# Optimization experiments

Hardware: AMD Instinct MI355X
Metric: run time of the kernel (lower is better)

The kernel has to match this reference:

```python
import jax, jax.numpy as jnp
import numpy as np

B, NNODE, D = 128, 64, 64          # graphs, nodes per graph, invariant feat dim
N = B * NNODE                      # 8192 nodes
E = B * NNODE * (NNODE - 1)        # 516096 directed edges (fully connected per graph)


def _silu(x):
    return x * jax.nn.sigmoid(x)


def _ln(x, w, b, eps=1e-5):
    mu = jnp.mean(x, axis=-1, keepdims=True)
    var = jnp.var(x, axis=-1, keepdims=True)
    return (x - mu) / jnp.sqrt(var + eps) * w + b


def setup_inputs() -> dict:
    key = jax.random.key(0)
    ks = jax.random.split(key, 12)
    # node -> graph assignment, sorted
    batch = np.repeat(np.arange(B), NNODE)
    # fully-connected directed edges within each graph (i != j)
    idx = np.arange(NNODE)
    s, d = np.meshgrid(idx, idx, indexing='ij')
    m = s != d
    s, d = s[m], d[m]
    off = (np.arange(B) * NNODE)[:, None]
    src = (s[None, :] + off).ravel()
    dst = (d[None, :] + off).ravel()
    E_idx = jnp.asarray(np.stack([src, dst]), dtype=jnp.int32)
    return dict(
        batch=jnp.asarray(batch, jnp.int32),
        X=jax.random.normal(ks[0], (N, 3), jnp.float32),
        H=jax.random.normal(ks[1], (N, D), jnp.float32),
        E_idx=E_idx,
        x_norm_w=jnp.ones((1, 1), jnp.float32),
        q_w1=jax.random.normal(ks[2], (D, D), jnp.float32) * 0.05,
        q_w2=jax.random.normal(ks[3], (D, D), jnp.float32) * 0.05,
        kv_w1=jax.random.normal(ks[4], (D + 1, 2 * D), jnp.float32) * 0.05,
        kv_w2=jax.random.normal(ks[5], (2 * D, 2 * D), jnp.float32) * 0.05,
        qn_w=jnp.ones((D,), jnp.float32), qn_b=jnp.zeros((D,), jnp.float32),
        kn_w=jnp.ones((D,), jnp.float32), kn_b=jnp.zeros((D,), jnp.float32),
        phx_w1=jax.random.normal(ks[6], (D, D), jnp.float32) * 0.05,
        phx_w2=jax.random.normal(ks[7], (D, 1), jnp.float32) * 0.05,
        phh_w1=jax.random.normal(ks[8], (D, D), jnp.float32) * 0.05,
        phh_b1=jnp.zeros((D,), jnp.float32),
        phh_w2=jax.random.normal(ks[9], (D, D), jnp.float32) * 0.05,
        phh_b2=jnp.zeros((D,), jnp.float32),
    )


def reference(batch, X, H, E_idx, x_norm_w, q_w1, q_w2, kv_w1, kv_w2,
              qn_w, qn_b, kn_w, kn_b, phx_w1, phx_w2,
              phh_w1, phh_b1, phh_w2, phh_b2):
    src, dst = E_idx[0], E_idx[1]
    # ---- E3Norm: scale positions by per-graph mean norm ----
    norm = jnp.linalg.norm(X, axis=-1, keepdims=True)                 # [N,1]
    cnt = jax.ops.segment_sum(jnp.ones((N,), X.dtype), batch, num_segments=B)
    mean_norm = jax.ops.segment_sum(norm, batch, num_segments=B) / cnt[:, None]
    Xn = x_norm_w * X / (mean_norm[batch] + 1e-5)                     # [N,3]
    # ---- edge gathers + MLPs ----
    Q = _silu(H[dst] @ q_w1) @ q_w2                                   # [E,D]
    rel = Xn[src] - Xn[dst]                                           # [E,3]
    rel_dist = jnp.sum(rel * rel, axis=-1, keepdims=True)             # [E,1]
    X_rel_norm = rel / (1.0 + jnp.sqrt(rel_dist + 1e-8))
    kv_in = jnp.concatenate([rel_dist, H[src]], axis=-1)              # [E,D+1]
    kv = _silu(kv_in @ kv_w1) @ kv_w2                                 # [E,2D]
    K, V = kv[:, :D], kv[:, D:]
    Q = _ln(Q, qn_w, qn_b)
    K = _ln(K, kn_w, kn_b)
    # ---- scatter softmax over incoming edges of dst ----
    scores = jnp.sum(Q * K, axis=-1) / jnp.sqrt(jnp.asarray(D, X.dtype))  # [E]
    m = jax.ops.segment_max(scores, dst, num_segments=N)
    e = jnp.exp(scores - m[dst])
    s = jax.ops.segment_sum(e, dst, num_segments=N)
    alpha = e / s[dst]                                                # [E]
    att = alpha[:, None] * V                                          # [E,D]
    # ---- scatter-sum aggregations ----
    A = jax.ops.segment_sum(att, dst, num_segments=N)                 # [N,D]
    AH = jax.ops.segment_sum(att * H[dst], dst, num_segments=N)       # [N,D]
    phx = _silu(att @ phx_w1) @ phx_w2                                # [E,1]
    X_out = Xn + jax.ops.segment_sum(X_rel_norm * phx, dst, num_segments=N)
    H_out = H + (_silu((A * AH) @ phh_w1 + phh_b1) @ phh_w2 + phh_b2)
    return X_out, H_out
```

## Files before the change

kernel.cpp:

```cpp
#include <hip/hip_runtime.h>
#include <math.h>

#define NB     128
#define NNODE  64
#define NTOT   8192
#define DIM    64
#define PSTR   136
#define WS72   72

typedef __bf16 bf16x8 __attribute__((ext_vector_type(8)));
typedef float  f32x4  __attribute__((ext_vector_type(4)));

__device__ __forceinline__ float frcp(float x) {
    return __builtin_amdgcn_rcpf(x);
}

__device__ __forceinline__ float silu_f(float x) {
    return x * frcp(1.0f + __expf(-x));
}

__device__ __forceinline__ unsigned short bf16bits(float f) {
    return __builtin_bit_cast(unsigned short, (__bf16)f);
}

__device__ __forceinline__ bf16x8 to_bf16x8(const float* v) {
    bf16x8 o;
    #pragma unroll
    for (int j = 0; j < 8; ++j) o[j] = (__bf16)v[j];
    return o;
}

__device__ __forceinline__ float wsum(float v) {
    #pragma unroll
    for (int m = 1; m < 64; m <<= 1) v += __shfl_xor(v, m, 64);
    return v;
}

template<int CTRL>
__device__ __forceinline__ float dpp_add(float v) {
    const int r = __builtin_amdgcn_update_dpp(
        0, __builtin_bit_cast(int, v), CTRL, 0xF, 0xF, true);
    return v + __builtin_bit_cast(float, r);
}
__device__ __forceinline__ float row_sum16(float v) {
    v = dpp_add<0x111>(v);
    v = dpp_add<0x112>(v);
    v = dpp_add<0x114>(v);
    v = dpp_add<0x118>(v);
    return v;
}
__device__ __forceinline__ float bcast15(float v) {
    return __builtin_bit_cast(float,
        __builtin_amdgcn_ds_swizzle(__builtin_bit_cast(int, v), 0x01F0));
}

__global__ __launch_bounds__(256) void k0_prep(
        const float* __restrict__ kvw2, const float* __restrict__ phxw1,
        const float* __restrict__ X, const float* __restrict__ xw,
        const float* __restrict__ qw1, const float* __restrict__ qw2,
        const float* __restrict__ kvw1,
        const float* __restrict__ phh1, const float* __restrict__ phh2,
        unsigned short* __restrict__ w2x, float* __restrict__ Xn4,
        unsigned short* __restrict__ qw1T, unsigned short* __restrict__ qw2T,
        unsigned short* __restrict__ kvw1T,
        unsigned short* __restrict__ phh1T, unsigned short* __restrict__ phh2T) {
    const int k = blockIdx.x;
    const int T = threadIdx.x;
    if (T < 128) {
        w2x[T*PSTR + k] = bf16bits(kvw2[k*128 + T]);
    } else if (T < 192) {
        const int n2 = T - 128;
        float acc = 0.f;
        #pragma unroll 8
        for (int j = 0; j < 64; ++j)
            acc += kvw2[k*128 + 64 + j] * phxw1[j*64 + n2];
        w2x[(128 + n2)*PSTR + k] = bf16bits(acc);
    } else {
        const int L = T - 192;
        const int n = k*64 + L;
        const float x0 = X[n*3+0], x1 = X[n*3+1], x2 = X[n*3+2];
        const float nm = sqrtf(x0*x0 + x1*x1 + x2*x2);
        const float mean = wsum(nm) * (1.0f/64.0f);
        const float sc = xw[0] * frcp(mean + 1e-5f);
        float4 o; o.x = x0*sc; o.y = x1*sc; o.z = x2*sc; o.w = 0.f;
        *(float4*)&Xn4[n*4] = o;
    }
    if (k < 64) {
        if (T < 128) kvw1T[T*WS72 + k] = bf16bits(kvw1[(1+k)*128 + T]);
    } else {
        const int kk = k - 64;
        if (T < 64)       qw1T[T*WS72 + kk]        = bf16bits(qw1[kk*64 + T]);
        else if (T < 128) qw2T[(T-64)*WS72 + kk]   = bf16bits(qw2[kk*64 + (T-64)]);
        else if (T < 192) phh1T[(T-128)*WS72 + kk] = bf16bits(phh1[kk*64 + (T-128)]);
        else              phh2T[(T-192)*WS72 + kk] = bf16bits(phh2[kk*64 + (T-192)]);
    }
}

__global__ __launch_bounds__(64) void k2_node(
        const float* __restrict__ H,
        const unsigned short* __restrict__ wbase,
        const float* __restrict__ qnw, const float* __restrict__ qnb,
        float* __restrict__ Qn, unsigned short* __restrict__ Ptb) {
    const int tile = blockIdx.x >> 1, role = blockIdx.x & 1;
    const int nb = tile * 16;
    const int L = threadIdx.x, q = L >> 4, m = L & 15;
    __shared__ __align__(16) unsigned short zb[16*WS72];

    bf16x8 hf[2];
    #pragma unroll
    for (int ks = 0; ks < 2; ++ks) {
        float v[8];
        *(float4*)&v[0] = *(const float4*)&H[(size_t)(nb + m)*64 + ks*32 + q*8];
        *(float4*)&v[4] = *(const float4*)&H[(size_t)(nb + m)*64 + ks*32 + q*8 + 4];
        hf[ks] = to_bf16x8(v);
    }

    f32x4 acc[4];
    if (role == 1) {
        const unsigned short* kvw1T = wbase + 128*WS72;
        #pragma unroll
        for (int ph = 0; ph < 2; ++ph) {
            #pragma unroll
            for (int ct = 0; ct < 4; ++ct) acc[ct] = (f32x4){0.f,0.f,0.f,0.f};
            #pragma unroll
            for (int ks = 0; ks < 2; ++ks)
                #pragma unroll
                for (int ct = 0; ct < 4; ++ct) {
                    const bf16x8 b = *(const bf16x8*)&kvw1T[(ph*64 + ct*16 + m)*WS72 + ks*32 + q*8];
                    acc[ct] = __builtin_amdgcn_mfma_f32_16x16x32_bf16(hf[ks], b, acc[ct], 0, 0, 0);
                }
            #pragma unroll
            for (int ct = 0; ct < 4; ++ct)
                #pragma unroll
                for (int r = 0; r < 4; ++r)
                    Ptb[(size_t)(nb + q*4 + r)*PSTR + ph*64 + ct*16 + m]
                        = bf16bits(acc[ct][r]);
        }
        return;
    }

    #pragma unroll
    for (int ct = 0; ct < 4; ++ct) acc[ct] = (f32x4){0.f,0.f,0.f,0.f};
    #pragma unroll
    for (int ks = 0; ks < 2; ++ks)
        #pragma unroll
        for (int ct = 0; ct < 4; ++ct) {
            const bf16x8 b = *(const bf16x8*)&wbase[(ct*16 + m)*WS72 + ks*32 + q*8];
            acc[ct] = __builtin_amdgcn_mfma_f32_16x16x32_bf16(hf[ks], b, acc[ct], 0, 0, 0);
        }
    #pragma unroll
    for (int ct = 0; ct < 4; ++ct)
        #pragma unroll
        for (int r = 0; r < 4; ++r)
            zb[(q*4 + r)*WS72 + ct*16 + m] = bf16bits(silu_f(acc[ct][r]));

    bf16x8 zf[2];
    #pragma unroll
    for (int ks = 0; ks < 2; ++ks)
        zf[ks] = *(const bf16x8*)&zb[m*WS72 + ks*32 + q*8];
    const unsigned short* qw2T = wbase + 64*WS72;
    #pragma unroll
    for (int ct = 0; ct < 4; ++ct) acc[ct] = (f32x4){0.f,0.f,0.f,0.f};
    #pragma unroll
    for (int ks = 0; ks < 2; ++ks)
        #pragma unroll
        for (int ct = 0; ct < 4; ++ct) {
            const bf16x8 b = *(const bf16x8*)&qw2T[(ct*16 + m)*WS72 + ks*32 + q*8];
            acc[ct] = __builtin_amdgcn_mfma_f32_16x16x32_bf16(zf[ks], b, acc[ct], 0, 0, 0);
        }
    float qnwv[4], qnbv[4];
    #pragma unroll
    for (int ct = 0; ct < 4; ++ct) { qnwv[ct] = qnw[ct*16+m]; qnbv[ct] = qnb[ct*16+m]; }
    #pragma unroll
    for (int r = 0; r < 4; ++r) {
        float s1 = 0.f, s2 = 0.f;
        #pragma unroll
        for (int ct = 0; ct < 4; ++ct) {
            const float z = acc[ct][r];
            s1 += z; s2 = fmaf(z, z, s2);
        }
        #pragma unroll
        for (int sh = 1; sh < 16; sh <<= 1) {
            s1 += __shfl_xor(s1, sh, 64);
            s2 += __shfl_xor(s2, sh, 64);
        }
        const float mu = s1 * (1.0f/64.0f);
        const float rstd = rsqrtf(s2 * (1.0f/64.0f) - mu*mu + 1e-5f);
        const int row = nb + q*4 + r;
        #pragma unroll
        for (int ct = 0; ct < 4; ++ct)
            Qn[(size_t)row*64 + ct*16 + m] = (acc[ct][r] - mu)*rstd*qnwv[ct] + qnbv[ct];
    }
}

__global__ __launch_bounds__(256, 3) void k3_edge(
        const float* __restrict__ Xn4, const float* __restrict__ Qn,
        const unsigned short* __restrict__ Ptb,
        const unsigned short* __restrict__ w2x,
        const float* __restrict__ kvw1,
        const float* __restrict__ knw, const float* __restrict__ knb,
        const float* __restrict__ pxw2,
        float* __restrict__ Abuf, float* __restrict__ Xout) {
    const int bid = blockIdx.x;
    const int g = bid >> 3, dgrp = bid & 7;
    const int T = threadIdx.x, w = T >> 6, L = T & 63;
    const int q = L >> 4, m = L & 15;
    const int pair = w >> 1, half = w & 1;

    __shared__ __align__(16) unsigned short sw2[128*PSTR];
    __shared__ __align__(16) float sXn[64][4];
    __shared__ __align__(16) float sQn[8][64];
    __shared__ __align__(16) float sxr[4][32][4];
    __shared__ float w0s[128];
    __shared__ float knws[64], knbs[64], pxs[64];
    __shared__ float sred[2][2][2];
    __shared__ float sA[2][64];
    __shared__ float sX[2][4];

    {
        const uint4* s1 = (const uint4*)w2x;
        uint4* d1 = (uint4*)sw2;
        #pragma unroll
        for (int it = 0; it < 9; ++it) {
            const int idx = T + 256*it;
            if (idx < 128*PSTR/8) d1[idx] = s1[idx];
        }
        const float* qsrc = Qn + ((size_t)g*64 + dgrp*8)*64;
        for (int idx = T; idx < 512; idx += 256)
            sQn[idx >> 6][idx & 63] = qsrc[idx];
        if (T < 64) *(float4*)&sXn[T][0] = *(const float4*)&Xn4[(g*64 + T)*4];
        if (T < 128) w0s[T] = kvw1[T];
        if (T < 64)            knws[T]       = knw[T];
        else if (T < 128)      knbs[T - 64]  = knb[T - 64];
        else if (T < 192)      pxs[T - 128]  = pxw2[T - 128];
    }
    __syncthreads();

    const unsigned short* PtG = Ptb + (size_t)g*64*PSTR;
    const unsigned short* Gw  = w2x + 128*PSTR;
    const float mflag = (m == 15) ? 1.0f : 0.0f;

    #pragma unroll 1
    for (int i = 0; i < 4; ++i) {
        const int dql = i*2 + pair;
        const int dl  = dgrp*8 + dql;
        const int d   = g*64 + dl;

        if (L < 32) {
            const int row = half*32 + L;
            const float4 xs  = *(const float4*)&sXn[row][0];
            const float4 xdv = *(const float4*)&sXn[dl][0];
            const float r0 = xs.x - xdv.x, r1 = xs.y - xdv.y, r2 = xs.z - xdv.z;
            const float rd = r0*r0 + r1*r1 + r2*r2;
            const float inv = frcp(1.0f + sqrtf(rd + 1e-8f));
            float4 o; o.x = r0*inv; o.y = r1*inv; o.z = r2*inv; o.w = rd;
            *(float4*)&sxr[w][L][0] = o;
        }
        asm volatile("s_waitcnt lgkmcnt(0)" ::: "memory");

        bf16x8 af[2][4];
        float rdv[2];
        #pragma unroll
        for (int rt = 0; rt < 2; ++rt) rdv[rt] = sxr[w][rt*16 + m][3];
        #pragma unroll
        for (int ks = 0; ks < 4; ++ks) {
            float w0v[8];
            *(float4*)&w0v[0] = *(const float4*)&w0s[ks*32 + q*8];
            *(float4*)&w0v[4] = *(const float4*)&w0s[ks*32 + q*8 + 4];
            #pragma unroll
            for (int rt = 0; rt < 2; ++rt) {
                const int row = half*32 + rt*16 + m;
                const bf16x8 pb = *(const bf16x8*)&PtG[(size_t)row*PSTR + ks*32 + q*8];
                bf16x8 o;
                #pragma unroll
                for (int j = 0; j < 8; ++j) {
                    const float pf = (float)pb[j];
                    o[j] = (__bf16)silu_f(fmaf(rdv[rt], w0v[j], pf));
                }
                af[rt][ks] = o;
            }
        }

        f32x4 acc[4][2];

        #pragma unroll
        for (int ct = 0; ct < 4; ++ct)
            #pragma unroll
            for (int rt = 0; rt < 2; ++rt)
                acc[ct][rt] = (f32x4){0.f, 0.f, 0.f, 0.f};
        #pragma unroll
        for (int ks = 0; ks < 4; ++ks)
            #pragma unroll
            for (int ct = 0; ct < 4; ++ct) {
                const bf16x8 b = *(const bf16x8*)&sw2[(ct*16 + m)*PSTR + ks*32 + q*8];
                #pragma unroll
                for (int rt = 0; rt < 2; ++rt)
                    acc[ct][rt] = __builtin_amdgcn_mfma_f32_16x16x32_bf16(
                                      af[rt][ks], b, acc[ct][rt], 0, 0, 0);
            }

        float qdw[4], Sqdw = 0.f, Sqdb = 0.f;
        #pragma unroll
        for (int ct = 0; ct < 4; ++ct) {
            const float qd = sQn[dql][ct*16 + m];
            qdw[ct] = qd * knws[ct*16 + m];
            Sqdw += qdw[ct];
            Sqdb += qd * knbs[ct*16 + m];
        }
        Sqdw = row_sum16(Sqdw);
        Sqdb = row_sum16(Sqdb);
        float sc[2][4];
        #pragma unroll
        for (int rt = 0; rt < 2; ++rt)
            #pragma unroll
            for (int r = 0; r < 4; ++r) {
                float s1 = 0.f, s2 = 0.f, skq = 0.f;
                #pragma unroll
                for (int ct = 0; ct < 4; ++ct) {
                    const float kv = acc[ct][rt][r];
                    s1 += kv; s2 = fmaf(kv, kv, s2); skq = fmaf(kv, qdw[ct], skq);
                }
                s1  = row_sum16(s1);
                s2  = row_sum16(s2);
                skq = row_sum16(skq);
                const float mu = s1 * (1.0f/64.0f);
                const float rstd = rsqrtf(s2 * (1.0f/64.0f) - mu*mu + 1e-5f);
                float scv = (rstd * (skq - mu*Sqdw) + Sqdb) * 0.125f;
                scv = bcast15(scv);
                const int row_g = half*32 + rt*16 + q*4 + r;
                sc[rt][r] = (row_g == dl) ? -1e30f : scv;
            }

        float mx = -1e30f;
        #pragma unroll
        for (int rt = 0; rt < 2; ++rt)
            #pragma unroll
            for (int r = 0; r < 4; ++r) mx = fmaxf(mx, sc[rt][r]);
        mx = fmaxf(mx, __shfl_xor(mx, 16, 64));
        mx = fmaxf(mx, __shfl_xor(mx, 32, 64));
        float al[2][4], S = 0.f;
        #pragma unroll
        for (int rt = 0; rt < 2; ++rt)
            #pragma unroll
            for (int r = 0; r < 4; ++r) {
                al[rt][r] = __expf(sc[rt][r] - mx);
                S += al[rt][r];
            }
        S += __shfl_xor(S, 16, 64);
        S += __shfl_xor(S, 32, 64);
        if (L == 0) { sred[pair][half][0] = mx; sred[pair][half][1] = S; }
        __syncthreads();
        {
            const float mo = sred[pair][half^1][0];
            const float So = sred[pair][half^1][1];
            const float M  = fmaxf(mx, mo);
            const float es = __expf(mx - M);
            const float eo = __expf(mo - M);
            const float alf = es * frcp(S*es + So*eo);
            #pragma unroll
            for (int rt = 0; rt < 2; ++rt)
                #pragma unroll
                for (int r = 0; r < 4; ++r) al[rt][r] *= alf;
        }

        #pragma unroll
        for (int ct = 0; ct < 4; ++ct)
            #pragma unroll
            for (int rt = 0; rt < 2; ++rt)
                acc[ct][rt] = (f32x4){0.f, 0.f, 0.f, 0.f};
        #pragma unroll
        for (int ks = 0; ks < 4; ++ks)
            #pragma unroll
            for (int ct = 0; ct < 4; ++ct) {
                const bf16x8 b = *(const bf16x8*)&sw2[(64 + ct*16 + m)*PSTR + ks*32 + q*8];
                #pragma unroll
                for (int rt = 0; rt < 2; ++rt)
                    acc[ct][rt] = __builtin_amdgcn_mfma_f32_16x16x32_bf16(
                                      af[rt][ks], b, acc[ct][rt], 0, 0, 0);
            }
        float p[4];
        #pragma unroll
        for (int ct = 0; ct < 4; ++ct) {
            float pv = 0.f;
            #pragma unroll
            for (int rt = 0; rt < 2; ++rt)
                #pragma unroll
                for (int r = 0; r < 4; ++r)
                    pv = fmaf(al[rt][r], acc[ct][rt][r], pv);
            pv += __shfl_xor(pv, 16, 64);
            pv += __shfl_xor(pv, 32, 64);
            p[ct] = pv;
        }

        #pragma unroll
        for (int ct = 0; ct < 4; ++ct)
            #pragma unroll
            for (int rt = 0; rt < 2; ++rt)
                acc[ct][rt] = (f32x4){0.f, 0.f, 0.f, 0.f};
        #pragma unroll
        for (int ks = 0; ks < 4; ++ks)
            #pragma unroll
            for (int ct = 0; ct < 4; ++ct) {
                const bf16x8 b = *(const bf16x8*)&Gw[(size_t)(ct*16 + m)*PSTR + ks*32 + q*8];
                #pragma unroll
                for (int rt = 0; rt < 2; ++rt)
                    acc[ct][rt] = __builtin_amdgcn_mfma_f32_16x16x32_bf16(
                                      af[rt][ks], b, acc[ct][rt], 0, 0, 0);
            }

        float pxc[4];
        #pragma unroll
        for (int ct = 0; ct < 4; ++ct) pxc[ct] = pxs[ct*16 + m];
        float xa0 = 0.f, xa1 = 0.f, xa2 = 0.f;
        #pragma unroll
        for (int rt = 0; rt < 2; ++rt)
            #pragma unroll
            for (int r = 0; r < 4; ++r) {
                float ph = 0.f;
                #pragma unroll
                for (int ct = 0; ct < 4; ++ct)
                    ph = fmaf(silu_f(al[rt][r] * acc[ct][rt][r]), pxc[ct], ph);
                ph = row_sum16(ph) * mflag;
                const float4 xr = *(const float4*)&sxr[w][rt*16 + q*4 + r][0];
                xa0 = fmaf(ph, xr.x, xa0);
                xa1 = fmaf(ph, xr.y, xa1);
                xa2 = fmaf(ph, xr.z, xa2);
            }
        xa0 += __shfl_xor(xa0, 16, 64); xa0 += __shfl_xor(xa0, 32, 64);
        xa1 += __shfl_xor(xa1, 16, 64); xa1 += __shfl_xor(xa1, 32, 64);
        xa2 += __shfl_xor(xa2, 16, 64); xa2 += __shfl_xor(xa2, 32, 64);

        if (half == 1) {
            if (q == 0)
                #pragma unroll
                for (int ct = 0; ct < 4; ++ct) sA[pair][ct*16 + m] = p[ct];
            if (L == 15) {
                sX[pair][0] = xa0; sX[pair][1] = xa1; sX[pair][2] = xa2;
            }
        }
        __syncthreads();
        if (half == 0) {
            if (q == 0)
                #pragma unroll
                for (int ct = 0; ct < 4; ++ct)
                    Abuf[(size_t)d*64 + ct*16 + m] = p[ct] + sA[pair][ct*16 + m];
            if (L == 15) {
                const float4 xdv = *(const float4*)&sXn[dl][0];
                Xout[(size_t)d*3 + 0] = xdv.x + xa0 + sX[pair][0];
                Xout[(size_t)d*3 + 1] = xdv.y + xa1 + sX[pair][1];
                Xout[(size_t)d*3 + 2] = xdv.z + xa2 + sX[pair][2];
            }
        }
    }
}

__global__ __launch_bounds__(64) void k4_hout(
        const float* __restrict__ H, const float* __restrict__ Abuf,
        const unsigned short* __restrict__ wbase,
        const float* __restrict__ b1, const float* __restrict__ b2,
        float* __restrict__ Hout) {
    const int nb = blockIdx.x * 16;
    const int L = threadIdx.x, q = L >> 4, m = L & 15;
    __shared__ __align__(16) unsigned short zb[16*WS72];

    bf16x8 uf[2];
    #pragma unroll
    for (int ks = 0; ks < 2; ++ks) {
        const size_t base = (size_t)(nb + m)*64 + ks*32 + q*8;
        float a[8], h[8], v[8];
        *(float4*)&a[0] = *(const float4*)&Abuf[base];
        *(float4*)&a[4] = *(const float4*)&Abuf[base + 4];
        *(float4*)&h[0] = *(const float4*)&H[base];
        *(float4*)&h[4] = *(const float4*)&H[base + 4];
        #pragma unroll
        for (int j = 0; j < 8; ++j) v[j] = a[j]*a[j]*h[j];
        uf[ks] = to_bf16x8(v);
    }

    f32x4 acc[4];
    #pragma unroll
    for (int ct = 0; ct < 4; ++ct) acc[ct] = (f32x4){0.f,0.f,0.f,0.f};
    #pragma unroll
    for (int ks = 0; ks < 2; ++ks)
        #pragma unroll
        for (int ct = 0; ct < 4; ++ct) {
            const bf16x8 b = *(const bf16x8*)&wbase[(ct*16 + m)*WS72 + ks*32 + q*8];
            acc[ct] = __builtin_amdgcn_mfma_f32_16x16x32_bf16(uf[ks], b, acc[ct], 0, 0, 0);
        }
    #pragma unroll
    for (int ct = 0; ct < 4; ++ct) {
        const float bv = b1[ct*16 + m];
        #pragma unroll
        for (int r = 0; r < 4; ++r)
            zb[(q*4 + r)*WS72 + ct*16 + m] = bf16bits(silu_f(acc[ct][r] + bv));
    }

    bf16x8 zf[2];
    #pragma unroll
    for (int ks = 0; ks < 2; ++ks)
        zf[ks] = *(const bf16x8*)&zb[m*WS72 + ks*32 + q*8];
    const unsigned short* phh2T = wbase + 64*WS72;
    #pragma unroll
    for (int ct = 0; ct < 4; ++ct) acc[ct] = (f32x4){0.f,0.f,0.f,0.f};
    #pragma unroll
    for (int ks = 0; ks < 2; ++ks)
        #pragma unroll
        for (int ct = 0; ct < 4; ++ct) {
            const bf16x8 b = *(const bf16x8*)&phh2T[(ct*16 + m)*WS72 + ks*32 + q*8];
            acc[ct] = __builtin_amdgcn_mfma_f32_16x16x32_bf16(zf[ks], b, acc[ct], 0, 0, 0);
        }
    #pragma unroll
    for (int ct = 0; ct < 4; ++ct) {
        const float bv = b2[ct*16 + m];
        #pragma unroll
        for (int r = 0; r < 4; ++r) {
            const size_t idx = (size_t)(nb + q*4 + r)*64 + ct*16 + m;
            Hout[idx] = H[idx] + acc[ct][r] + bv;
        }
    }
}

extern "C" void kernel_launch(void* const* d_in, const int* in_sizes, int n_in,
                              void* d_out, int out_size, void* d_ws, size_t ws_size,
                              hipStream_t stream) {
    const float* X    = (const float*)d_in[1];
    const float* H    = (const float*)d_in[2];
    const float* xw   = (const float*)d_in[4];
    const float* qw1  = (const float*)d_in[5];
    const float* qw2  = (const float*)d_in[6];
    const float* kvw1 = (const float*)d_in[7];
    const float* kvw2 = (const float*)d_in[8];
    const float* qnw  = (const float*)d_in[9];
    const float* qnb  = (const float*)d_in[10];
    const float* knw  = (const float*)d_in[11];
    const float* knb  = (const float*)d_in[12];
    const float* pxw1 = (const float*)d_in[13];
    const float* pxw2 = (const float*)d_in[14];
    const float* phw1 = (const float*)d_in[15];
    const float* phb1 = (const float*)d_in[16];
    const float* phw2 = (const float*)d_in[17];
    const float* phb2 = (const float*)d_in[18];

    float* out = (float*)d_out;
    char*  ws  = (char*)d_ws;

    size_t off = 0;
    float* Xn4 = (float*)(ws + off);          off += (size_t)NTOT*4*4;
    float* Qn  = (float*)(ws + off);          off += (size_t)NTOT*64*4;
    unsigned short* Ptb = (unsigned short*)(ws + off); off += (size_t)NTOT*PSTR*2;
    float* Ab  = (float*)(ws + off);          off += (size_t)NTOT*64*4;
    unsigned short* w2x   = (unsigned short*)(ws + off); off += (size_t)192*PSTR*2;
    unsigned short* qw1T  = (unsigned short*)(ws + off); off += (size_t)64*WS72*2;
    unsigned short* qw2T  = (unsigned short*)(ws + off); off += (size_t)64*WS72*2;
    unsigned short* kvw1T = (unsigned short*)(ws + off); off += (size_t)128*WS72*2;
    unsigned short* phh1T = (unsigned short*)(ws + off); off += (size_t)64*WS72*2;
    unsigned short* phh2T = (unsigned short*)(ws + off); off += (size_t)64*WS72*2;

    k0_prep<<<128, 256, 0, stream>>>(kvw2, pxw1, X, xw, qw1, qw2, kvw1,
                                     phw1, phw2, w2x, Xn4,
                                     qw1T, qw2T, kvw1T, phh1T, phh2T);
    k2_node<<<1024, 64, 0, stream>>>(H, qw1T, qnw, qnb, Qn, Ptb);
    k3_edge<<<1024, 256, 0, stream>>>(Xn4, Qn, Ptb, w2x, kvw1, knw, knb,
                                      pxw2, Ab, out);
    k4_hout<<<512, 64, 0, stream>>>(H, Ab, phh1T, phb1, phb2, out + NTOT*3);
}
```

Before: 173.1 us.

## Fuse H-output MLP into edge kernel and restructure MFMA accumulators per column tile

Removes the separate k4_hout kernel: each edge block keeps its 8 aggregated A rows in shared memory as bf16 and runs the phh MLP with one wave after a block barrier, so the global A buffer round trip and one launch disappear. The three MFMA stages now loop per column tile with a small accumulator and fold reductions in immediately, which cuts register pressure and allows launch bounds of 4 blocks. The Qn and Xn shared staging is dropped in favour of direct global loads. The added tail wastes half of a wave (q<2) and serialises on one wave, and A is now rounded to bf16 before squaring.

```diff
diff --git a/kernel.cpp b/kernel.cpp
--- a/kernel.cpp
+++ b/kernel.cpp
@@ -193,14 +193,17 @@
     }
 }
 
-__global__ __launch_bounds__(256, 3) void k3_edge(
+__global__ __launch_bounds__(256, 4) void k3_edge(
         const float* __restrict__ Xn4, const float* __restrict__ Qn,
         const unsigned short* __restrict__ Ptb,
         const unsigned short* __restrict__ w2x,
         const float* __restrict__ kvw1,
         const float* __restrict__ knw, const float* __restrict__ knb,
         const float* __restrict__ pxw2,
-        float* __restrict__ Abuf, float* __restrict__ Xout) {
+        const unsigned short* __restrict__ phhT,
+        const float* __restrict__ phb1, const float* __restrict__ phb2,
+        const float* __restrict__ H,
+        float* __restrict__ Hout, float* __restrict__ Xout) {
     const int bid = blockIdx.x;
     const int g = bid >> 3, dgrp = bid & 7;
     const int T = threadIdx.x, w = T >> 6, L = T & 63;
@@ -208,9 +211,8 @@
     const int pair = w >> 1, half = w & 1;
 
     __shared__ __align__(16) unsigned short sw2[128*PSTR];
-    __shared__ __align__(16) float sXn[64][4];
-    __shared__ __align__(16) float sQn[8][64];
     __shared__ __align__(16) float sxr[4][32][4];
+    __shared__ __align__(16) unsigned short sAb[8*WS72];
     __shared__ float w0s[128];
     __shared__ float knws[64], knbs[64], pxs[64];
     __shared__ float sred[2][2][2];
@@ -225,10 +227,6 @@
             const int idx = T + 256*it;
             if (idx < 128*PSTR/8) d1[idx] = s1[idx];
         }
-        const float* qsrc = Qn + ((size_t)g*64 + dgrp*8)*64;
-        for (int idx = T; idx < 512; idx += 256)
-            sQn[idx >> 6][idx & 63] = qsrc[idx];
-        if (T < 64) *(float4*)&sXn[T][0] = *(const float4*)&Xn4[(g*64 + T)*4];
         if (T < 128) w0s[T] = kvw1[T];
         if (T < 64)            knws[T]       = knw[T];
         else if (T < 128)      knbs[T - 64]  = knb[T - 64];
@@ -246,10 +244,15 @@
         const int dl  = dgrp*8 + dql;
         const int d   = g*64 + dl;
 
+        float qdv[4];
+        #pragma unroll
+        for (int ct = 0; ct < 4; ++ct)
+            qdv[ct] = Qn[(size_t)d*64 + ct*16 + m];
+
         if (L < 32) {
             const int row = half*32 + L;
-            const float4 xs  = *(const float4*)&sXn[row][0];
-            const float4 xdv = *(const float4*)&sXn[dl][0];
+            const float4 xs  = *(const float4*)&Xn4[(g*64 + row)*4];
+            const float4 xdv = *(const float4*)&Xn4[(g*64 + dl)*4];
             const float r0 = xs.x - xdv.x, r1 = xs.y - xdv.y, r2 = xs.z - xdv.z;
             const float rd = r0*r0 + r1*r1 + r2*r2;
             const float inv = frcp(1.0f + sqrtf(rd + 1e-8f));
@@ -281,48 +284,54 @@
             }
         }
 
-        f32x4 acc[4][2];
-
-        #pragma unroll
-        for (int ct = 0; ct < 4; ++ct)
-            #pragma unroll
-            for (int rt = 0; rt < 2; ++rt)
-                acc[ct][rt] = (f32x4){0.f, 0.f, 0.f, 0.f};
-        #pragma unroll
-        for (int ks = 0; ks < 4; ++ks)
-            #pragma unroll
-            for (int ct = 0; ct < 4; ++ct) {
-                const bf16x8 b = *(const bf16x8*)&sw2[(ct*16 + m)*PSTR + ks*32 + q*8];
-                #pragma unroll
-                for (int rt = 0; rt < 2; ++rt)
-                    acc[ct][rt] = __builtin_amdgcn_mfma_f32_16x16x32_bf16(
-                                      af[rt][ks], b, acc[ct][rt], 0, 0, 0);
-            }
-
         float qdw[4], Sqdw = 0.f, Sqdb = 0.f;
         #pragma unroll
         for (int ct = 0; ct < 4; ++ct) {
-            const float qd = sQn[dql][ct*16 + m];
-            qdw[ct] = qd * knws[ct*16 + m];
+            qdw[ct] = qdv[ct] * knws[ct*16 + m];
             Sqdw += qdw[ct];
-            Sqdb += qd * knbs[ct*16 + m];
+            Sqdb += qdv[ct] * knbs[ct*16 + m];
         }
         Sqdw = row_sum16(Sqdw);
         Sqdb = row_sum16(Sqdb);
+
+        float s1a[2][4], s2a[2][4], skqa[2][4];
+        #pragma unroll
+        for (int rt = 0; rt < 2; ++rt)
+            #pragma unroll
+            for (int r = 0; r < 4; ++r) { s1a[rt][r]=0.f; s2a[rt][r]=0.f; skqa[rt][r]=0.f; }
+
+        #pragma unroll
+        for (int ct = 0; ct < 4; ++ct) {
+            f32x4 acc[2];
+            acc[0] = (f32x4){0.f,0.f,0.f,0.f};
+            acc[1] = (f32x4){0.f,0.f,0.f,0.f};
+            #pragma unroll
+            for (int ks = 0; ks < 4; ++ks) {
+                const bf16x8 b = *(const bf16x8*)&sw2[(ct*16 + m)*PSTR + ks*32 + q*8];
+                #pragma unroll
+                for (int rt = 0; rt < 2; ++rt)
+                    acc[rt] = __builtin_amdgcn_mfma_f32_16x16x32_bf16(
+                                  af[rt][ks], b, acc[rt], 0, 0, 0);
+            }
+            #pragma unroll
+            for (int rt = 0; rt < 2; ++rt)
+                #pragma unroll
+                for (int r = 0; r < 4; ++r) {
+                    const float kv = acc[rt][r];
+                    s1a[rt][r] += kv;
+                    s2a[rt][r] = fmaf(kv, kv, s2a[rt][r]);
+                    skqa[rt][r] = fmaf(kv, qdw[ct], skqa[rt][r]);
+                }
+        }
+
         float sc[2][4];
         #pragma unroll
         for (int rt = 0; rt < 2; ++rt)
             #pragma unroll
             for (int r = 0; r < 4; ++r) {
-                float s1 = 0.f, s2 = 0.f, skq = 0.f;
-                #pragma unroll
-                for (int ct = 0; ct < 4; ++ct) {
-                    const float kv = acc[ct][rt][r];
-                    s1 += kv; s2 = fmaf(kv, kv, s2); skq = fmaf(kv, qdw[ct], skq);
-                }
-                s1  = row_sum16(s1);
-                s2  = row_sum16(s2);
-                skq = row_sum16(skq);
+                const float s1 = row_sum16(s1a[rt][r]);
+                const float s2 = row_sum16(s2a[rt][r]);
+                const float skq = row_sum16(skqa[rt][r]);
                 const float mu = s1 * (1.0f/64.0f);
                 const float rstd = rsqrtf(s2 * (1.0f/64.0f) - mu*mu + 1e-5f);
                 float scv = (rstd * (skq - mu*Sqdw) + Sqdb) * 0.125f;
@@ -363,64 +372,63 @@
                 for (int r = 0; r < 4; ++r) al[rt][r] *= alf;
         }
 
-        #pragma unroll
-        for (int ct = 0; ct < 4; ++ct)
+        float p[4];
+        #pragma unroll
+        for (int ct = 0; ct < 4; ++ct) {
+            f32x4 acc[2];
+            acc[0] = (f32x4){0.f,0.f,0.f,0.f};
+            acc[1] = (f32x4){0.f,0.f,0.f,0.f};
+            #pragma unroll
+            for (int ks = 0; ks < 4; ++ks) {
+                const bf16x8 b = *(const bf16x8*)&sw2[(64 + ct*16 + m)*PSTR + ks*32 + q*8];
+                #pragma unroll
+                for (int rt = 0; rt < 2; ++rt)
+                    acc[rt] = __builtin_amdgcn_mfma_f32_16x16x32_bf16(
+                                  af[rt][ks], b, acc[rt], 0, 0, 0);
+            }
+            float pv = 0.f;
             #pragma unroll
             for (int rt = 0; rt < 2; ++rt)
-                acc[ct][rt] = (f32x4){0.f, 0.f, 0.f, 0.f};
-        #pragma unroll
-        for (int ks = 0; ks < 4; ++ks)
-            #pragma unroll
-            for (int ct = 0; ct < 4; ++ct) {
-                const bf16x8 b = *(const bf16x8*)&sw2[(64 + ct*16 + m)*PSTR + ks*32 + q*8];
-                #pragma unroll
-                for (int rt = 0; rt < 2; ++rt)
-                    acc[ct][rt] = __builtin_amdgcn_mfma_f32_16x16x32_bf16(
-                                      af[rt][ks], b, acc[ct][rt], 0, 0, 0);
-            }
-        float p[4];
-        #pragma unroll
-        for (int ct = 0; ct < 4; ++ct) {
-            float pv = 0.f;
-            #pragma unroll
-            for (int rt = 0; rt < 2; ++rt)
                 #pragma unroll
                 for (int r = 0; r < 4; ++r)
-                    pv = fmaf(al[rt][r], acc[ct][rt][r], pv);
+                    pv = fmaf(al[rt][r], acc[rt][r], pv);
             pv += __shfl_xor(pv, 16, 64);
             pv += __shfl_xor(pv, 32, 64);
             p[ct] = pv;
         }
 
-        #pragma unroll
-        for (int ct = 0; ct < 4; ++ct)
+        float phsum[2][4];
+        #pragma unroll
+        for (int rt = 0; rt < 2; ++rt)
+            #pragma unroll
+            for (int r = 0; r < 4; ++r) phsum[rt][r] = 0.f;
+        #pragma unroll
+        for (int ct = 0; ct < 4; ++ct) {
+            f32x4 acc[2];
+            acc[0] = (f32x4){0.f,0.f,0.f,0.f};
+            acc[1] = (f32x4){0.f,0.f,0.f,0.f};
+            #pragma unroll
+            for (int ks = 0; ks < 4; ++ks) {
+                const bf16x8 b = *(const bf16x8*)&Gw[(size_t)(ct*16 + m)*PSTR + ks*32 + q*8];
+                #pragma unroll
+                for (int rt = 0; rt < 2; ++rt)
+                    acc[rt] = __builtin_amdgcn_mfma_f32_16x16x32_bf16(
+                                  af[rt][ks], b, acc[rt], 0, 0, 0);
+            }
+            const float px = pxs[ct*16 + m];
             #pragma unroll
             for (int rt = 0; rt < 2; ++rt)
-                acc[ct][rt] = (f32x4){0.f, 0.f, 0.f, 0.f};
-        #pragma unroll
-        for (int ks = 0; ks < 4; ++ks)
-            #pragma unroll
-            for (int ct = 0; ct < 4; ++ct) {
-                const bf16x8 b = *(const bf16x8*)&Gw[(size_t)(ct*16 + m)*PSTR + ks*32 + q*8];
-                #pragma unroll
-                for (int rt = 0; rt < 2; ++rt)
-                    acc[ct][rt] = __builtin_amdgcn_mfma_f32_16x16x32_bf16(
-                                      af[rt][ks], b, acc[ct][rt], 0, 0, 0);
-            }
-
-        float pxc[4];
-        #pragma unroll
-        for (int ct = 0; ct < 4; ++ct) pxc[ct] = pxs[ct*16 + m];
+                #pragma unroll
+                for (int r = 0; r < 4; ++r)
+                    phsum[rt][r] = fmaf(silu_f(al[rt][r] * acc[rt][r]), px, phsum[rt][r]);
+        }
+
         float xa0 = 0.f, xa1 = 0.f, xa2 = 0.f;
         #pragma unroll
         for (int rt = 0; rt < 2; ++rt)
             #pragma unroll
             for (int r = 0; r < 4; ++r) {
-                float ph = 0.f;
-                #pragma unroll
-                for (int ct = 0; ct < 4; ++ct)
-                    ph = fmaf(silu_f(al[rt][r] * acc[ct][rt][r]), pxc[ct], ph);
-                ph = row_sum16(ph) * mflag;
+                const float ph = row_sum16(phsum[rt][r]) * mflag;
                 const float4 xr = *(const float4*)&sxr[w][rt*16 + q*4 + r][0];
                 xa0 = fmaf(ph, xr.x, xa0);
                 xa1 = fmaf(ph, xr.y, xa1);
@@ -443,79 +451,79 @@
             if (q == 0)
                 #pragma unroll
                 for (int ct = 0; ct < 4; ++ct)
-                    Abuf[(size_t)d*64 + ct*16 + m] = p[ct] + sA[pair][ct*16 + m];
+                    sAb[dql*WS72 + ct*16 + m] =
+                        bf16bits(p[ct] + sA[pair][ct*16 + m]);
             if (L == 15) {
-                const float4 xdv = *(const float4*)&sXn[dl][0];
+                const float4 xdv = *(const float4*)&Xn4[(g*64 + dl)*4];
                 Xout[(size_t)d*3 + 0] = xdv.x + xa0 + sX[pair][0];
                 Xout[(size_t)d*3 + 1] = xdv.y + xa1 + sX[pair][1];
                 Xout[(size_t)d*3 + 2] = xdv.z + xa2 + sX[pair][2];
             }
         }
     }
-}
-
-__global__ __launch_bounds__(64) void k4_hout(
-        const float* __restrict__ H, const float* __restrict__ Abuf,
-        const unsigned short* __restrict__ wbase,
-        const float* __restrict__ b1, const float* __restrict__ b2,
-        float* __restrict__ Hout) {
-    const int nb = blockIdx.x * 16;
-    const int L = threadIdx.x, q = L >> 4, m = L & 15;
-    __shared__ __align__(16) unsigned short zb[16*WS72];
-
-    bf16x8 uf[2];
-    #pragma unroll
-    for (int ks = 0; ks < 2; ++ks) {
-        const size_t base = (size_t)(nb + m)*64 + ks*32 + q*8;
-        float a[8], h[8], v[8];
-        *(float4*)&a[0] = *(const float4*)&Abuf[base];
-        *(float4*)&a[4] = *(const float4*)&Abuf[base + 4];
-        *(float4*)&h[0] = *(const float4*)&H[base];
-        *(float4*)&h[4] = *(const float4*)&H[base + 4];
-        #pragma unroll
-        for (int j = 0; j < 8; ++j) v[j] = a[j]*a[j]*h[j];
-        uf[ks] = to_bf16x8(v);
-    }
-
-    f32x4 acc[4];
-    #pragma unroll
-    for (int ct = 0; ct < 4; ++ct) acc[ct] = (f32x4){0.f,0.f,0.f,0.f};
-    #pragma unroll
-    for (int ks = 0; ks < 2; ++ks)
-        #pragma unroll
-        for (int ct = 0; ct < 4; ++ct) {
-            const bf16x8 b = *(const bf16x8*)&wbase[(ct*16 + m)*WS72 + ks*32 + q*8];
-            acc[ct] = __builtin_amdgcn_mfma_f32_16x16x32_bf16(uf[ks], b, acc[ct], 0, 0, 0);
-        }
-    #pragma unroll
-    for (int ct = 0; ct < 4; ++ct) {
-        const float bv = b1[ct*16 + m];
-        #pragma unroll
-        for (int r = 0; r < 4; ++r)
-            zb[(q*4 + r)*WS72 + ct*16 + m] = bf16bits(silu_f(acc[ct][r] + bv));
-    }
-
-    bf16x8 zf[2];
-    #pragma unroll
-    for (int ks = 0; ks < 2; ++ks)
-        zf[ks] = *(const bf16x8*)&zb[m*WS72 + ks*32 + q*8];
-    const unsigned short* phh2T = wbase + 64*WS72;
-    #pragma unroll
-    for (int ct = 0; ct < 4; ++ct) acc[ct] = (f32x4){0.f,0.f,0.f,0.f};
-    #pragma unroll
-    for (int ks = 0; ks < 2; ++ks)
-        #pragma unroll
-        for (int ct = 0; ct < 4; ++ct) {
-            const bf16x8 b = *(const bf16x8*)&phh2T[(ct*16 + m)*WS72 + ks*32 + q*8];
-            acc[ct] = __builtin_amdgcn_mfma_f32_16x16x32_bf16(zf[ks], b, acc[ct], 0, 0, 0);
-        }
-    #pragma unroll
-    for (int ct = 0; ct < 4; ++ct) {
-        const float bv = b2[ct*16 + m];
-        #pragma unroll
-        for (int r = 0; r < 4; ++r) {
-            const size_t idx = (size_t)(nb + q*4 + r)*64 + ct*16 + m;
-            Hout[idx] = H[idx] + acc[ct][r] + bv;
+
+    __syncthreads();
+    if (w == 0) {
+        const int mr = m & 7;
+        const size_t nbase = (size_t)g*64 + dgrp*8;
+
+        bf16x8 uf[2];
+        #pragma unroll
+        for (int ks = 0; ks < 2; ++ks) {
+            const bf16x8 a8 = *(const bf16x8*)&sAb[mr*WS72 + ks*32 + q*8];
+            float h[8], v[8];
+            *(float4*)&h[0] = *(const float4*)&H[(nbase + mr)*64 + ks*32 + q*8];
+            *(float4*)&h[4] = *(const float4*)&H[(nbase + mr)*64 + ks*32 + q*8 + 4];
+            #pragma unroll
+            for (int j = 0; j < 8; ++j) {
+                const float a = (float)a8[j];
+                v[j] = a * a * h[j];
+            }
+            uf[ks] = to_bf16x8(v);
+        }
+
+        f32x4 acc[4];
+        #pragma unroll
+        for (int ct = 0; ct < 4; ++ct) acc[ct] = (f32x4){0.f,0.f,0.f,0.f};
+        #pragma unroll
+        for (int ks = 0; ks < 2; ++ks)
+            #pragma unroll
+            for (int ct = 0; ct < 4; ++ct) {
+                const bf16x8 b = *(const bf16x8*)&phhT[(ct*16 + m)*WS72 + ks*32 + q*8];
+                acc[ct] = __builtin_amdgcn_mfma_f32_16x16x32_bf16(uf[ks], b, acc[ct], 0, 0, 0);
+            }
+        #pragma unroll
+        for (int ct = 0; ct < 4; ++ct) {
+            const float bv = phb1[ct*16 + m];
+            #pragma unroll
+            for (int r = 0; r < 4; ++r)
+                if (q < 2)
+                    sAb[(q*4 + r)*WS72 + ct*16 + m] = bf16bits(silu_f(acc[ct][r] + bv));
+        }
+
+        bf16x8 zf[2];
+        #pragma unroll
+        for (int ks = 0; ks < 2; ++ks)
+            zf[ks] = *(const bf16x8*)&sAb[mr*WS72 + ks*32 + q*8];
+        const unsigned short* phh2T = phhT + 64*WS72;
+        #pragma unroll
+        for (int ct = 0; ct < 4; ++ct) acc[ct] = (f32x4){0.f,0.f,0.f,0.f};
+        #pragma unroll
+        for (int ks = 0; ks < 2; ++ks)
+            #pragma unroll
+            for (int ct = 0; ct < 4; ++ct) {
+                const bf16x8 b = *(const bf16x8*)&phh2T[(ct*16 + m)*WS72 + ks*32 + q*8];
+                acc[ct] = __builtin_amdgcn_mfma_f32_16x16x32_bf16(zf[ks], b, acc[ct], 0, 0, 0);
+            }
+        #pragma unroll
+        for (int ct = 0; ct < 4; ++ct) {
+            const float bv = phb2[ct*16 + m];
+            #pragma unroll
+            for (int r = 0; r < 4; ++r)
+                if (q < 2) {
+                    const size_t idx = (nbase + q*4 + r)*64 + ct*16 + m;
+                    Hout[idx] = H[idx] + acc[ct][r] + bv;
+                }
         }
     }
 }
@@ -548,7 +556,6 @@
     float* Xn4 = (float*)(ws + off);          off += (size_t)NTOT*4*4;
     float* Qn  = (float*)(ws + off);          off += (size_t)NTOT*64*4;
     unsigned short* Ptb = (unsigned short*)(ws + off); off += (size_t)NTOT*PSTR*2;
-    float* Ab  = (float*)(ws + off);          off += (size_t)NTOT*64*4;
     unsigned short* w2x   = (unsigned short*)(ws + off); off += (size_t)192*PSTR*2;
     unsigned short* qw1T  = (unsigned short*)(ws + off); off += (size_t)64*WS72*2;
     unsigned short* qw2T  = (unsigned short*)(ws + off); off += (size_t)64*WS72*2;
@@ -561,6 +568,6 @@
                                      qw1T, qw2T, kvw1T, phh1T, phh2T);
     k2_node<<<1024, 64, 0, stream>>>(H, qw1T, qnw, qnb, Qn, Ptb);
     k3_edge<<<1024, 256, 0, stream>>>(Xn4, Qn, Ptb, w2x, kvw1, knw, knb,
-                                      pxw2, Ab, out);
-    k4_hout<<<512, 64, 0, stream>>>(H, Ab, phh1T, phb1, phb2, out + NTOT*3);
-}
+                                      pxw2, phh1T, phb1, phb2, H,
+                                      out + NTOT*3, out);
+}
```

New measurement: 165.5 us. 4.4% less time.
